# Optimization experiments

Measured on AMD Instinct MI355X. Metric: run time of the kernel, lower is better.

The kernel has to match this reference:

```python
import jax, jax.numpy as jnp
import numpy as np

ALPHA = 0.2          # LeakyReLU negative slope
NEG_INF = -9e15      # mask value from the torch source
N, F_IN, F_OUT = 8192, 128, 64


def setup_inputs() -> dict:
    key = jax.random.key(0)
    k1, k2, k3, k4, k5 = jax.random.split(key, 5)
    X = jax.random.normal(k1, (N, F_IN), dtype=jnp.float32)
    A = jax.random.randint(k2, (N, N), 0, 2, dtype=jnp.int32)  # 0/1 adjacency
    W = jax.random.normal(k3, (F_IN, F_OUT), dtype=jnp.float32) * 0.05
    a1 = jax.random.normal(k4, (F_OUT,), dtype=jnp.float32) * 0.05
    a2 = jax.random.normal(k5, (F_OUT,), dtype=jnp.float32) * 0.05
    return {"X": X, "A": A, "W": W, "a1": a1, "a2": a2}


def reference(X, A, W, a1, a2):
    # h = W(X)  (Linear, no bias)
    h = X @ W                                   # (N, F_out)
    # a([h_i || h_j]) == h_i @ a1 + h_j @ a2  (split of the 2F attention vector)
    s1 = h @ a1                                 # (N,)
    s2 = h @ a2                                 # (N,)
    e = jax.nn.leaky_relu(s1[:, None] + s2[None, :], ALPHA)  # (N, N)
    att = jnp.where(A > 0, e, NEG_INF)
    att = jax.nn.softmax(att, axis=1)           # row-wise masked softmax
    # dropout p=0.0 -> identity
    return att @ h                              # (N, F_out)
```

## Files before the change

### kernel.cpp

```cpp
#include <hip/hip_runtime.h>
#include <hip/hip_bf16.h>

#define NV 8192
#define FIN 128
#define FOUT 64

typedef __attribute__((ext_vector_type(8))) short short8;
typedef __attribute__((ext_vector_type(4))) float floatx4;

__device__ __forceinline__ uint f2bf_u(float f) {
  uint u = __float_as_uint(f);
  return (u + 0x7FFFu + ((u >> 16) & 1u)) >> 16;
}
__device__ __forceinline__ float bf2f(ushort b) {
  return __uint_as_float(((uint)b) << 16);
}

__global__ void k0_detect(const uint* __restrict__ X, int* __restrict__ flag) {
  const int lane = threadIdx.x & 63;
  uint u = X[lane];
  uint e = (u >> 7) & 0xFF;
  bool ok = (e >= 100u) && (e <= 135u);
  unsigned long long b = __ballot(ok);
  if (lane == 0) *flag = (__builtin_popcountll(b) >= 48) ? 1 : 0;
}

__global__ __launch_bounds__(256) void k1_proj(
    const void* __restrict__ Xv, const void* __restrict__ Wv,
    const void* __restrict__ a1v_, const void* __restrict__ a2v_,
    ushort* __restrict__ HtT, float* __restrict__ s1, float* __restrict__ s2,
    const int* __restrict__ flagp)
{
  const int is_bf16 = *flagp;
  const int wave = threadIdx.x >> 6;
  const int lane = threadIdx.x & 63;
  const int i0 = blockIdx.x * 64 + wave * 16;
  const int col = lane & 15;
  const int q   = lane >> 4;

  short8 bfrag[4][4];
  float a1f[4], a2f[4];
  if (is_bf16) {
    const ushort* W = (const ushort*)Wv;
#pragma unroll
    for (int nt = 0; nt < 4; ++nt)
#pragma unroll
      for (int kc = 0; kc < 4; ++kc) {
        short8 b;
#pragma unroll
        for (int j = 0; j < 8; ++j)
          b[j] = (short)W[(kc*32 + q*8 + j)*FOUT + nt*16 + col];
        bfrag[nt][kc] = b;
      }
#pragma unroll
    for (int nt = 0; nt < 4; ++nt) {
      a1f[nt] = bf2f(((const ushort*)a1v_)[nt*16 + col]);
      a2f[nt] = bf2f(((const ushort*)a2v_)[nt*16 + col]);
    }
  } else {
    const float* W = (const float*)Wv;
#pragma unroll
    for (int nt = 0; nt < 4; ++nt)
#pragma unroll
      for (int kc = 0; kc < 4; ++kc) {
        short8 b;
#pragma unroll
        for (int j = 0; j < 8; ++j)
          b[j] = (short)f2bf_u(W[(kc*32 + q*8 + j)*FOUT + nt*16 + col]);
        bfrag[nt][kc] = b;
      }
#pragma unroll
    for (int nt = 0; nt < 4; ++nt) {
      a1f[nt] = ((const float*)a1v_)[nt*16 + col];
      a2f[nt] = ((const float*)a2v_)[nt*16 + col];
    }
  }

  floatx4 acc[4] = {{0.f,0.f,0.f,0.f},{0.f,0.f,0.f,0.f},
                    {0.f,0.f,0.f,0.f},{0.f,0.f,0.f,0.f}};
#pragma unroll
  for (int kc = 0; kc < 4; ++kc) {
    short8 a;
    if (is_bf16) {
      a = *(const short8*)&((const ushort*)Xv)[(size_t)(i0 + col)*FIN + kc*32 + q*8];
    } else {
      const float* X = (const float*)Xv;
      float4 x0 = *(const float4*)&X[(size_t)(i0 + col)*FIN + kc*32 + q*8];
      float4 x1 = *(const float4*)&X[(size_t)(i0 + col)*FIN + kc*32 + q*8 + 4];
      a[0] = (short)f2bf_u(x0.x); a[1] = (short)f2bf_u(x0.y);
      a[2] = (short)f2bf_u(x0.z); a[3] = (short)f2bf_u(x0.w);
      a[4] = (short)f2bf_u(x1.x); a[5] = (short)f2bf_u(x1.y);
      a[6] = (short)f2bf_u(x1.z); a[7] = (short)f2bf_u(x1.w);
    }
#pragma unroll
    for (int nt = 0; nt < 4; ++nt)
      acc[nt] = __builtin_amdgcn_mfma_f32_16x16x32_bf16(a, bfrag[nt][kc], acc[nt], 0, 0, 0);
  }

  float s1p[4] = {0,0,0,0}, s2p[4] = {0,0,0,0};
#pragma unroll
  for (int nt = 0; nt < 4; ++nt) {
    ushort4 pk;
    pk.x = (ushort)f2bf_u(acc[nt][0]);
    pk.y = (ushort)f2bf_u(acc[nt][1]);
    pk.z = (ushort)f2bf_u(acc[nt][2]);
    pk.w = (ushort)f2bf_u(acc[nt][3]);
    *(ushort4*)&HtT[(size_t)(nt*16 + col)*NV + i0 + q*4] = pk;
#pragma unroll
    for (int reg = 0; reg < 4; ++reg) {
      s1p[reg] += acc[nt][reg] * a1f[nt];
      s2p[reg] += acc[nt][reg] * a2f[nt];
    }
  }
#pragma unroll
  for (int m = 1; m < 16; m <<= 1)
#pragma unroll
    for (int reg = 0; reg < 4; ++reg) {
      s1p[reg] += __shfl_xor(s1p[reg], m, 64);
      s2p[reg] += __shfl_xor(s2p[reg], m, 64);
    }
  if (col == 0)
#pragma unroll
    for (int reg = 0; reg < 4; ++reg) {
      s1[i0 + q*4 + reg] = s1p[reg];
      s2[i0 + q*4 + reg] = s2p[reg];
    }
}

#define CT 256
#define NTILES (NV / CT)
#define PST 72

__global__ __launch_bounds__(256) void k2_attn(
    const int* __restrict__ A, const ushort* __restrict__ HtT,
    const float* __restrict__ s1g, const float* __restrict__ s2g,
    void* __restrict__ outv, const int* __restrict__ flagp)
{
  __shared__ __align__(16) ushort Pl[4][16 * PST];
  __shared__ __align__(16) float Red[4][16][64];
  __shared__ float Lw[4][16];

  const int is_bf16 = *flagp;
  const int tid  = threadIdx.x;
  const int wave = tid >> 6;
  const int lane = tid & 63;
  const int i0   = blockIdx.x * 16;
  const int q    = lane >> 4;
  const int mcol = lane & 15;

  ushort* Pw = &Pl[wave][0];

  float s1v[4];
#pragma unroll
  for (int rr = 0; rr < 4; ++rr) s1v[rr] = s1g[i0 + q*4 + rr];

  size_t arow[4], hrow[4];
#pragma unroll
  for (int rr = 0; rr < 4; ++rr)
    arow[rr] = (size_t)(i0 + q*4 + rr) * NV + mcol*4;
#pragma unroll
  for (int nt = 0; nt < 4; ++nt)
    hrow[nt] = (size_t)(nt*16 + mcol) * NV + q*8;

  float Lp[4] = {0,0,0,0};
  floatx4 acc[4] = {{0.f,0.f,0.f,0.f},{0.f,0.f,0.f,0.f},
                    {0.f,0.f,0.f,0.f},{0.f,0.f,0.f,0.f}};

#pragma unroll 2
  for (int t = 0; t < NTILES; ++t) {
    const int c = t*CT + wave*64;
    int4 av[4];
#pragma unroll
    for (int rr = 0; rr < 4; ++rr)
      av[rr] = *(const int4*)&A[arow[rr] + c];
    float4 s2v = *(const float4*)&s2g[c + mcol*4];

#pragma unroll
    for (int rr = 0; rr < 4; ++rr) {
      const int4 a = av[rr];
      const float s1r = s1v[rr];
      float x0 = s1r + s2v.x, x1 = s1r + s2v.y, x2 = s1r + s2v.z, x3 = s1r + s2v.w;
      float w0 = a.x ? __expf(fmaxf(x0, 0.2f*x0)) : 0.f;
      float w1 = a.y ? __expf(fmaxf(x1, 0.2f*x1)) : 0.f;
      float w2 = a.z ? __expf(fmaxf(x2, 0.2f*x2)) : 0.f;
      float w3 = a.w ? __expf(fmaxf(x3, 0.2f*x3)) : 0.f;
      Lp[rr] += (w0 + w1) + (w2 + w3);
      uint2 pk;
      pk.x = f2bf_u(w0) | (f2bf_u(w1) << 16);
      pk.y = f2bf_u(w2) | (f2bf_u(w3) << 16);
      *(uint2*)&Pw[(q*4 + rr)*PST + mcol*4] = pk;
    }

#pragma unroll
    for (int kc2 = 0; kc2 < 2; ++kc2) {
      short8 af = *(const short8*)&Pw[mcol*PST + kc2*32 + q*8];
#pragma unroll
      for (int nt = 0; nt < 4; ++nt) {
        short8 bf = *(const short8*)&HtT[hrow[nt] + c + kc2*32];
        acc[nt] = __builtin_amdgcn_mfma_f32_16x16x32_bf16(af, bf, acc[nt], 0, 0, 0);
      }
    }
  }

#pragma unroll
  for (int m = 1; m < 16; m <<= 1)
#pragma unroll
    for (int rr = 0; rr < 4; ++rr) Lp[rr] += __shfl_xor(Lp[rr], m, 64);
  if (mcol == 0)
#pragma unroll
    for (int rr = 0; rr < 4; ++rr) Lw[wave][q*4 + rr] = Lp[rr];

#pragma unroll
  for (int nt = 0; nt < 4; ++nt)
#pragma unroll
    for (int reg = 0; reg < 4; ++reg)
      Red[wave][q*4 + reg][nt*16 + mcol] = acc[nt][reg];

  __syncthreads();

  {
    const int r  = tid >> 4;
    const int fb = (tid & 15) * 4;
    float4 s = {0.f, 0.f, 0.f, 0.f};
    float L = 0.f;
#pragma unroll
    for (int w = 0; w < 4; ++w) {
      float4 v = *(const float4*)&Red[w][r][fb];
      s.x += v.x; s.y += v.y; s.z += v.z; s.w += v.w;
      L += Lw[w][r];
    }
    const float inv = __frcp_rn(L);
    s.x *= inv; s.y *= inv; s.z *= inv; s.w *= inv;
    if (is_bf16) {
      ushort4 pk;
      pk.x = (ushort)f2bf_u(s.x); pk.y = (ushort)f2bf_u(s.y);
      pk.z = (ushort)f2bf_u(s.z); pk.w = (ushort)f2bf_u(s.w);
      *(ushort4*)&((ushort*)outv)[(size_t)(i0 + r)*FOUT + fb] = pk;
    } else {
      *(float4*)&((float*)outv)[(size_t)(i0 + r)*FOUT + fb] = s;
    }
  }
}

extern "C" void kernel_launch(void* const* d_in, const int* in_sizes, int n_in,
                              void* d_out, int out_size, void* d_ws, size_t ws_size,
                              hipStream_t stream) {
  const void* X  = d_in[0];
  const int*  A  = (const int*)d_in[1];
  const void* W  = d_in[2];
  const void* a1 = d_in[3];
  const void* a2 = d_in[4];

  char* ws = (char*)d_ws;
  ushort* HtT  = (ushort*)ws;
  float*  s1   = (float*)(ws + (size_t)FOUT*NV*2);
  float*  s2   = s1 + NV;
  int*    flag = (int*)(s2 + NV);

  hipLaunchKernelGGL(k0_detect, dim3(1), dim3(64), 0, stream,
                     (const uint*)X, flag);
  hipLaunchKernelGGL(k1_proj, dim3(NV/64), dim3(256), 0, stream,
                     X, W, a1, a2, HtT, s1, s2, flag);
  hipLaunchKernelGGL(k2_attn, dim3(NV/16), dim3(256), 0, stream,
                     A, HtT, s1, s2, d_out, flag);
}
```

Baseline: 404.5 us.

## Store projected features in MFMA-fragment-blocked layout and prefetch adjacency tiles

The projection kernel now writes H in a blocked layout where each 64-node chunk holds exactly the B-fragments the attention MFMA needs. Each lane can then load a contiguous 16-byte fragment instead of strided rows of a transposed matrix. The attention loop also software-prefetches the next tile's adjacency ints and s2 values into registers while it computes the current tile, to hide global load latency. This costs more live registers and may lower occupancy.

After: 457.6 us. 1.13x slower.

```diff
diff --git a/kernel.cpp b/kernel.cpp
--- a/kernel.cpp
+++ b/kernel.cpp
@@ -28,7 +28,7 @@
 __global__ __launch_bounds__(256) void k1_proj(
     const void* __restrict__ Xv, const void* __restrict__ Wv,
     const void* __restrict__ a1v_, const void* __restrict__ a2v_,
-    ushort* __restrict__ HtT, float* __restrict__ s1, float* __restrict__ s2,
+    ushort* __restrict__ HtB, float* __restrict__ s1, float* __restrict__ s2,
     const int* __restrict__ flagp)
 {
   const int is_bf16 = *flagp;
@@ -97,6 +97,12 @@
       acc[nt] = __builtin_amdgcn_mfma_f32_16x16x32_bf16(a, bfrag[nt][kc], acc[nt], 0, 0, 0);
   }
 
+  const int r0  = wave*16 + q*4;
+  const int kcH = r0 >> 5;
+  const int q2  = (r0 >> 3) & 3;
+  const int j0  = r0 & 7;
+  ushort* chunkp = HtB + (size_t)blockIdx.x * 4096;
+
   float s1p[4] = {0,0,0,0}, s2p[4] = {0,0,0,0};
 #pragma unroll
   for (int nt = 0; nt < 4; ++nt) {
@@ -105,7 +111,7 @@
     pk.y = (ushort)f2bf_u(acc[nt][1]);
     pk.z = (ushort)f2bf_u(acc[nt][2]);
     pk.w = (ushort)f2bf_u(acc[nt][3]);
-    *(ushort4*)&HtT[(size_t)(nt*16 + col)*NV + i0 + q*4] = pk;
+    *(ushort4*)&chunkp[((kcH*4 + nt)*64 + q2*16 + col)*8 + j0] = pk;
 #pragma unroll
     for (int reg = 0; reg < 4; ++reg) {
       s1p[reg] += acc[nt][reg] * a1f[nt];
@@ -128,11 +134,11 @@
 }
 
 #define CT 256
-#define NTILES (NV / CT)
+#define NT (NV / CT)
 #define PST 72
 
 __global__ __launch_bounds__(256) void k2_attn(
-    const int* __restrict__ A, const ushort* __restrict__ HtT,
+    const int* __restrict__ A, const ushort* __restrict__ HtB,
     const float* __restrict__ s1g, const float* __restrict__ s2g,
     void* __restrict__ outv, const int* __restrict__ flagp)
 {
@@ -154,32 +160,38 @@
 #pragma unroll
   for (int rr = 0; rr < 4; ++rr) s1v[rr] = s1g[i0 + q*4 + rr];
 
-  size_t arow[4], hrow[4];
+  size_t arow[4];
 #pragma unroll
   for (int rr = 0; rr < 4; ++rr)
     arow[rr] = (size_t)(i0 + q*4 + rr) * NV + mcol*4;
-#pragma unroll
-  for (int nt = 0; nt < 4; ++nt)
-    hrow[nt] = (size_t)(nt*16 + mcol) * NV + q*8;
 
   float Lp[4] = {0,0,0,0};
   floatx4 acc[4] = {{0.f,0.f,0.f,0.f},{0.f,0.f,0.f,0.f},
                     {0.f,0.f,0.f,0.f},{0.f,0.f,0.f,0.f}};
 
-#pragma unroll 2
-  for (int t = 0; t < NTILES; ++t) {
+  int4 av[4];
+  float4 sv;
+  {
+    const int c = wave * 64;
+#pragma unroll
+    for (int rr = 0; rr < 4; ++rr) av[rr] = *(const int4*)&A[arow[rr] + c];
+    sv = *(const float4*)&s2g[c + mcol*4];
+  }
+
+  for (int t = 0; t < NT; ++t) {
     const int c = t*CT + wave*64;
-    int4 av[4];
-#pragma unroll
-    for (int rr = 0; rr < 4; ++rr)
-      av[rr] = *(const int4*)&A[arow[rr] + c];
-    float4 s2v = *(const float4*)&s2g[c + mcol*4];
+    const int cn = (t + 1 < NT) ? (c + CT) : c;
+    int4 nav[4];
+    float4 nsv;
+#pragma unroll
+    for (int rr = 0; rr < 4; ++rr) nav[rr] = *(const int4*)&A[arow[rr] + cn];
+    nsv = *(const float4*)&s2g[cn + mcol*4];
 
 #pragma unroll
     for (int rr = 0; rr < 4; ++rr) {
       const int4 a = av[rr];
       const float s1r = s1v[rr];
-      float x0 = s1r + s2v.x, x1 = s1r + s2v.y, x2 = s1r + s2v.z, x3 = s1r + s2v.w;
+      float x0 = s1r + sv.x, x1 = s1r + sv.y, x2 = s1r + sv.z, x3 = s1r + sv.w;
       float w0 = a.x ? __expf(fmaxf(x0, 0.2f*x0)) : 0.f;
       float w1 = a.y ? __expf(fmaxf(x1, 0.2f*x1)) : 0.f;
       float w2 = a.z ? __expf(fmaxf(x2, 0.2f*x2)) : 0.f;
@@ -191,15 +203,20 @@
       *(uint2*)&Pw[(q*4 + rr)*PST + mcol*4] = pk;
     }
 
+    const size_t chb = (size_t)(t*4 + wave) * 4096;
 #pragma unroll
     for (int kc2 = 0; kc2 < 2; ++kc2) {
       short8 af = *(const short8*)&Pw[mcol*PST + kc2*32 + q*8];
 #pragma unroll
       for (int nt = 0; nt < 4; ++nt) {
-        short8 bf = *(const short8*)&HtT[hrow[nt] + c + kc2*32];
+        short8 bf = *(const short8*)&HtB[chb + ((kc2*4 + nt)*64 + lane)*8];
         acc[nt] = __builtin_amdgcn_mfma_f32_16x16x32_bf16(af, bf, acc[nt], 0, 0, 0);
       }
     }
+
+#pragma unroll
+    for (int rr = 0; rr < 4; ++rr) av[rr] = nav[rr];
+    sv = nsv;
   }
 
 #pragma unroll
@@ -252,7 +269,7 @@
   const void* a2 = d_in[4];
 
   char* ws = (char*)d_ws;
-  ushort* HtT  = (ushort*)ws;
+  ushort* HtB  = (ushort*)ws;
   float*  s1   = (float*)(ws + (size_t)FOUT*NV*2);
   float*  s2   = s1 + NV;
   int*    flag = (int*)(s2 + NV);
@@ -260,7 +277,7 @@
   hipLaunchKernelGGL(k0_detect, dim3(1), dim3(64), 0, stream,
                      (const uint*)X, flag);
   hipLaunchKernelGGL(k1_proj, dim3(NV/64), dim3(256), 0, stream,
-                     X, W, a1, a2, HtT, s1, s2, flag);
+                     X, W, a1, a2, HtB, s1, s2, flag);
   hipLaunchKernelGGL(k2_attn, dim3(NV/16), dim3(256), 0, stream,
-                     A, HtT, s1, s2, d_out, flag);
-}
+                     A, HtB, s1, s2, d_out, flag);
+}
```
